# Optimization experiments

Measured on AMD Instinct MI355X. Metric: run time of the kernel, lower is better.

Reference implementation:

```python
import jax, jax.numpy as jnp
import numpy as np

B, N, GN, GS = 16, 100000, 4096, 64  # batch, points, num_groups, group_size


def setup_inputs() -> dict:
    key = jax.random.key(0)
    k1, k2, k3 = jax.random.split(key, 3)
    x_proto = jax.random.normal(k1, (B, N, 3), dtype=jnp.float32)
    template = jax.random.normal(k2, (N, 3), dtype=jnp.float32)
    groups = jax.random.randint(k3, (GN, GS), 0, N, dtype=jnp.int32)
    return {"x_proto": x_proto, "template": template, "groups": groups}


def reference(x_proto, template, groups):
    # x_proto: [B, N, 3], template: [N, 3], groups: [GN, GS] int indices
    b, n, _ = x_proto.shape
    Yg = template[groups]                      # [GN, GS, 3] gathered template
    Xg = x_proto[:, groups]                    # [B, GN, GS, 3] gathered current points

    # Kabsch: align template group Y to current X (R @ Y + t ~ X)
    muY = Yg.mean(axis=1)                      # [GN, 3]
    muX = Xg.mean(axis=2)                      # [B, GN, 3]
    Yc = Yg - muY[:, None, :]
    Xc = Xg - muX[:, :, None, :]
    H = jnp.einsum('gni,bgnj->bgij', Yc, Xc)   # [B, GN, 3, 3] covariance
    U, S, Vh = jnp.linalg.svd(H)
    V = jnp.swapaxes(Vh, -2, -1)
    R0 = V @ jnp.swapaxes(U, -2, -1)
    det = jnp.linalg.det(R0)                   # [B, GN]
    # flip last column of V where det < 0 to get a proper rotation
    s = jnp.where(det < 0, -1.0, 1.0).astype(x_proto.dtype)
    col_scale = jnp.stack([jnp.ones_like(s), jnp.ones_like(s), s], axis=-1)  # [B, GN, 3]
    R = (V * col_scale[..., None, :]) @ jnp.swapaxes(U, -2, -1)              # [B, GN, 3, 3]
    t = muX - jnp.einsum('bgij,gj->bgi', R, muY)                             # [B, GN, 3]

    # project template group through (R, t)
    Xg_proj = jnp.einsum('bgij,gnj->bgni', R, Yg) + t[:, :, None, :]         # [B, GN, GS, 3]

    # scatter-add with overlap counting, then average
    flat_idx = groups.reshape(-1)              # [GN*GS]
    out = jnp.zeros_like(x_proto).at[:, flat_idx].add(Xg_proj.reshape(b, -1, 3))
    counts = jnp.zeros((n,), dtype=x_proto.dtype).at[flat_idx].add(1.0)
    counts = jnp.maximum(counts, 1.0)
    return out / counts[None, :, None]
```

## Files before the change

kernel.cpp:

```cpp
#include <hip/hip_runtime.h>
#include <math.h>

static constexpr int BB = 16;
static constexpr int NN = 100000;
static constexpr int GN = 4096;
static constexpr int GS = 64;
static constexpr int NP = BB * GN;
static constexpr int NE = GN * GS;
static constexpr int NBLK = (NN + 255) / 256;

__device__ __forceinline__ float wsum64(float v) {
#pragma unroll
  for (int off = 32; off > 0; off >>= 1) v += __shfl_xor(v, off, 64);
  return v;
}

__global__ __launch_bounds__(256) void k_tpl(
    const float* __restrict__ tpl, const int* __restrict__ groups,
    float* __restrict__ Yg, float* __restrict__ GmY, int* __restrict__ cnt) {
  int g    = blockIdx.x * 4 + (threadIdx.x >> 6);
  int lane = threadIdx.x & 63;
  int idx = groups[g * GS + lane];
  atomicAdd(&cnt[idx], 1);
  float y0 = tpl[idx * 3 + 0], y1 = tpl[idx * 3 + 1], y2 = tpl[idx * 3 + 2];
  float* o = Yg + ((size_t)g * GS + lane) * 3;
  o[0] = y0; o[1] = y1; o[2] = y2;
  float sy0 = wsum64(y0), sy1 = wsum64(y1), sy2 = wsum64(y2);
  if (lane == 0) {
    const float inv = 1.0f / 64.0f;
    float4 m = make_float4(sy0 * inv, sy1 * inv, sy2 * inv, 0.0f);
    *(float4*)(GmY + (size_t)g * 4) = m;
  }
}

__global__ __launch_bounds__(256) void k_stats(
    const float* __restrict__ x, const float* __restrict__ Yg,
    const float* __restrict__ GmY, const int* __restrict__ groups,
    float* __restrict__ Ht) {
  int wid4 = blockIdx.x * 4 + (threadIdx.x >> 6);
  int lane = threadIdx.x & 63;
  int s    = lane >> 4;
  int l4   = lane & 15;
  int p = wid4 * 4 + s;
  int b = p >> 12;
  int g = p & (GN - 1);

  int4 iv = *(const int4*)(groups + (size_t)g * GS + l4 * 4);
  const float4* yv = (const float4*)(Yg + ((size_t)g * GS + l4 * 4) * 3);
  float4 ya = yv[0], yb = yv[1], yc = yv[2];

  const float* xb = x + (size_t)b * NN * 3;
  float sx0 = 0.f, sx1 = 0.f, sx2 = 0.f;
  float h00 = 0.f, h01 = 0.f, h02 = 0.f;
  float h10 = 0.f, h11 = 0.f, h12 = 0.f;
  float h20 = 0.f, h21 = 0.f, h22 = 0.f;

#define ACC(Y0, Y1, Y2, IDX)                                   \
  {                                                            \
    const float* xp = xb + (size_t)(IDX) * 3;                  \
    float x0 = xp[0], x1 = xp[1], x2 = xp[2];                  \
    sx0 += x0; sx1 += x1; sx2 += x2;                           \
    h00 += (Y0) * x0; h01 += (Y0) * x1; h02 += (Y0) * x2;      \
    h10 += (Y1) * x0; h11 += (Y1) * x1; h12 += (Y1) * x2;      \
    h20 += (Y2) * x0; h21 += (Y2) * x1; h22 += (Y2) * x2;      \
  }
  ACC(ya.x, ya.y, ya.z, iv.x);
  ACC(ya.w, yb.x, yb.y, iv.y);
  ACC(yb.z, yb.w, yc.x, iv.z);
  ACC(yc.y, yc.z, yc.w, iv.w);
#undef ACC

#define RED(V)                                                 \
  V += __shfl_xor(V, 8, 64); V += __shfl_xor(V, 4, 64);        \
  V += __shfl_xor(V, 2, 64); V += __shfl_xor(V, 1, 64);
  RED(sx0) RED(sx1) RED(sx2)
  RED(h00) RED(h01) RED(h02)
  RED(h10) RED(h11) RED(h12)
  RED(h20) RED(h21) RED(h22)
#undef RED

  if (l4 == 0) {
    const float inv = 1.0f / 64.0f;
    float4 m = *(const float4*)(GmY + (size_t)g * 4);
    float mx0 = sx0 * inv, mx1 = sx1 * inv, mx2 = sx2 * inv;
    float4 o0 = make_float4(mx0, mx1, mx2, h00 - m.x * sx0);
    float4 o1 = make_float4(h01 - m.x * sx1, h02 - m.x * sx2,
                            h10 - m.y * sx0, h11 - m.y * sx1);
    float4 o2 = make_float4(h12 - m.y * sx2, h20 - m.z * sx0,
                            h21 - m.z * sx1, h22 - m.z * sx2);
    float* o = Ht + (size_t)p * 12;
    *(float4*)(o + 0) = o0;
    *(float4*)(o + 4) = o1;
    *(float4*)(o + 8) = o2;
  }
}

#define JROT(P, Q, RR)                                                        \
  {                                                                           \
    float apq = K[P][Q];                                                      \
    if (fabsf(apq) > 1e-30f) {                                                \
      float app = K[P][P], aqq = K[Q][Q];                                     \
      float tau = (aqq - app) / (2.0f * apq);                                 \
      float tt = copysignf(1.0f, tau) / (fabsf(tau) + sqrtf(1.0f + tau*tau)); \
      float cc = 1.0f / sqrtf(1.0f + tt * tt);                                \
      float ss = tt * cc;                                                     \
      K[P][P] = app - tt * apq;                                               \
      K[Q][Q] = aqq + tt * apq;                                               \
      K[P][Q] = 0.0f; K[Q][P] = 0.0f;                                         \
      float krp = K[RR][P], krq = K[RR][Q];                                   \
      K[RR][P] = cc * krp - ss * krq; K[P][RR] = K[RR][P];                    \
      K[RR][Q] = ss * krp + cc * krq; K[Q][RR] = K[RR][Q];                    \
      float v0p = V[0][P], v0q = V[0][Q];                                     \
      float v1p = V[1][P], v1q = V[1][Q];                                     \
      float v2p = V[2][P], v2q = V[2][Q];                                     \
      V[0][P] = cc * v0p - ss * v0q; V[0][Q] = ss * v0p + cc * v0q;           \
      V[1][P] = cc * v1p - ss * v1q; V[1][Q] = ss * v1p + cc * v1q;           \
      V[2][P] = cc * v2p - ss * v2q; V[2][Q] = ss * v2p + cc * v2q;           \
    }                                                                         \
  }

#define FIN(AA, BBi, CC)                                                      \
  {                                                                           \
    float va0 = V[0][AA], va1 = V[1][AA], va2 = V[2][AA];                     \
    float vb0 = V[0][BBi], vb1 = V[1][BBi], vb2 = V[2][BBi];                  \
    float vc0 = V[0][CC], vc1 = V[1][CC], vc2 = V[2][CC];                     \
    float ua0 = A[0][0]*va0 + A[0][1]*va1 + A[0][2]*va2;                      \
    float ua1 = A[1][0]*va0 + A[1][1]*va1 + A[1][2]*va2;                      \
    float ua2 = A[2][0]*va0 + A[2][1]*va1 + A[2][2]*va2;                      \
    float il = 1.0f / sqrtf(ua0*ua0 + ua1*ua1 + ua2*ua2 + 1e-30f);            \
    ua0 *= il; ua1 *= il; ua2 *= il;                                          \
    float ub0 = A[0][0]*vb0 + A[0][1]*vb1 + A[0][2]*vb2;                      \
    float ub1 = A[1][0]*vb0 + A[1][1]*vb1 + A[1][2]*vb2;                      \
    float ub2 = A[2][0]*vb0 + A[2][1]*vb1 + A[2][2]*vb2;                      \
    il = 1.0f / sqrtf(ub0*ub0 + ub1*ub1 + ub2*ub2 + 1e-30f);                  \
    ub0 *= il; ub1 *= il; ub2 *= il;                                          \
    float dd = ua0*ub0 + ua1*ub1 + ua2*ub2;                                   \
    ub0 -= dd * ua0; ub1 -= dd * ua1; ub2 -= dd * ua2;                        \
    il = 1.0f / sqrtf(ub0*ub0 + ub1*ub1 + ub2*ub2 + 1e-30f);                  \
    ub0 *= il; ub1 *= il; ub2 *= il;                                          \
    float uc0 = ua1*ub2 - ua2*ub1;                                            \
    float uc1 = ua2*ub0 - ua0*ub2;                                            \
    float uc2 = ua0*ub1 - ua1*ub0;                                            \
    R[0][0] = va0*ua0 + vb0*ub0 + dsg*vc0*uc0;                                \
    R[0][1] = va0*ua1 + vb0*ub1 + dsg*vc0*uc1;                                \
    R[0][2] = va0*ua2 + vb0*ub2 + dsg*vc0*uc2;                                \
    R[1][0] = va1*ua0 + vb1*ub0 + dsg*vc1*uc0;                                \
    R[1][1] = va1*ua1 + vb1*ub1 + dsg*vc1*uc1;                                \
    R[1][2] = va1*ua2 + vb1*ub2 + dsg*vc1*uc2;                                \
    R[2][0] = va2*ua0 + vb2*ub0 + dsg*vc2*uc0;                                \
    R[2][1] = va2*ua1 + vb2*ub1 + dsg*vc2*uc1;                                \
    R[2][2] = va2*ua2 + vb2*ub2 + dsg*vc2*uc2;                                \
  }

__global__ __launch_bounds__(256) void k_svd(
    const float* __restrict__ Ht, const float* __restrict__ GmY,
    float* __restrict__ Rt) {
  int p = blockIdx.x * 256 + threadIdx.x;
  if (p >= NP) return;
  int g = p & (GN - 1);
  const float* h = Ht + (size_t)p * 12;
  float4 f0 = *(const float4*)(h + 0);
  float4 f1 = *(const float4*)(h + 4);
  float4 f2 = *(const float4*)(h + 8);
  float4 m  = *(const float4*)(GmY + (size_t)g * 4);
  float mx0 = f0.x, mx1 = f0.y, mx2 = f0.z;
  float my0 = m.x, my1 = m.y, my2 = m.z;
  float A[3][3];
  A[0][0] = f0.w; A[0][1] = f1.x; A[0][2] = f1.y;
  A[1][0] = f1.z; A[1][1] = f1.w; A[1][2] = f2.x;
  A[2][0] = f2.y; A[2][1] = f2.z; A[2][2] = f2.w;

  float K[3][3];
#pragma unroll
  for (int i = 0; i < 3; ++i)
#pragma unroll
    for (int j = 0; j < 3; ++j)
      K[i][j] = A[0][i]*A[0][j] + A[1][i]*A[1][j] + A[2][i]*A[2][j];

  float V[3][3] = {{1.f,0.f,0.f},{0.f,1.f,0.f},{0.f,0.f,1.f}};
#pragma unroll
  for (int sweep = 0; sweep < 5; ++sweep) {
    JROT(0, 1, 2);
    JROT(0, 2, 1);
    JROT(1, 2, 0);
  }

  float d0 = K[0][0], d1 = K[1][1], d2 = K[2][2];
  float detV = V[0][0]*(V[1][1]*V[2][2] - V[1][2]*V[2][1])
             - V[0][1]*(V[1][0]*V[2][2] - V[1][2]*V[2][0])
             + V[0][2]*(V[1][0]*V[2][1] - V[1][1]*V[2][0]);
  float dsg = (detV < 0.0f) ? -1.0f : 1.0f;

  float R[3][3];
  if (d0 <= d1 && d0 <= d2) {
    FIN(1, 2, 0);
  } else if (d1 <= d0 && d1 <= d2) {
    FIN(2, 0, 1);
  } else {
    FIN(0, 1, 2);
  }

  float t0 = mx0 - (R[0][0]*my0 + R[0][1]*my1 + R[0][2]*my2);
  float t1 = mx1 - (R[1][0]*my0 + R[1][1]*my1 + R[1][2]*my2);
  float t2 = mx2 - (R[2][0]*my0 + R[2][1]*my1 + R[2][2]*my2);

  float* o = Rt + (size_t)p * 12;
  o[0] = R[0][0]; o[1] = R[0][1]; o[2] = R[0][2];
  o[3] = R[1][0]; o[4] = R[1][1]; o[5] = R[1][2];
  o[6] = R[2][0]; o[7] = R[2][1]; o[8] = R[2][2];
  o[9] = t0; o[10] = t1; o[11] = t2;
}

__global__ __launch_bounds__(256) void k_scan1(
    const int* __restrict__ cnt, int* __restrict__ blockSums) {
  __shared__ int lds[4];
  int t = blockIdx.x * 256 + threadIdx.x;
  int v = (t < NN) ? cnt[t] : 0;
#pragma unroll
  for (int off = 32; off > 0; off >>= 1) v += __shfl_xor(v, off, 64);
  if ((threadIdx.x & 63) == 0) lds[threadIdx.x >> 6] = v;
  __syncthreads();
  if (threadIdx.x == 0)
    blockSums[blockIdx.x] = lds[0] + lds[1] + lds[2] + lds[3];
}

__global__ __launch_bounds__(512) void k_scan2(int* __restrict__ blockSums) {
  __shared__ int lds[512];
  int tid = threadIdx.x;
  int v = (tid < NBLK) ? blockSums[tid] : 0;
  lds[tid] = v;
  __syncthreads();
#pragma unroll
  for (int off = 1; off < 512; off <<= 1) {
    int add = (tid >= off) ? lds[tid - off] : 0;
    __syncthreads();
    lds[tid] += add;
    __syncthreads();
  }
  if (tid < NBLK) blockSums[tid] = lds[tid] - v;
}

__global__ __launch_bounds__(256) void k_scan3(
    const int* __restrict__ cnt, const int* __restrict__ blockSums,
    int* __restrict__ row_start, int* __restrict__ cursor) {
  __shared__ int lds[256];
  int tid = threadIdx.x;
  int t = blockIdx.x * 256 + tid;
  int v = (t < NN) ? cnt[t] : 0;
  lds[tid] = v;
  __syncthreads();
#pragma unroll
  for (int off = 1; off < 256; off <<= 1) {
    int add = (tid >= off) ? lds[tid - off] : 0;
    __syncthreads();
    lds[tid] += add;
    __syncthreads();
  }
  if (t < NN) {
    row_start[t] = lds[tid] - v + blockSums[blockIdx.x];
    cursor[t] = 0;
  }
}

__global__ __launch_bounds__(256) void k_fill(
    const int* __restrict__ groups, const int* __restrict__ row_start,
    int* __restrict__ cursor, unsigned* __restrict__ entries) {
  int e = blockIdx.x * 256 + threadIdx.x;
  if (e >= NE) return;
  int n = groups[e];
  int pos = atomicAdd(&cursor[n], 1);
  entries[row_start[n] + pos] = (unsigned)(e >> 6);
}

__global__ __launch_bounds__(256) void k_gather(
    const float* __restrict__ tpl, const int* __restrict__ row_start,
    const int* __restrict__ cnt, const unsigned* __restrict__ entries,
    const float* __restrict__ Rt, float* __restrict__ out) {
  int n = blockIdx.x * 256 + threadIdx.x;
  if (n >= NN) return;
  int b = blockIdx.y;
  int s = row_start[n];
  int c = cnt[n];
  float y0 = tpl[n * 3 + 0], y1 = tpl[n * 3 + 1], y2 = tpl[n * 3 + 2];
  float p0 = 0.f, p1 = 0.f, p2 = 0.f;
  for (int j = 0; j < c; ++j) {
    unsigned g = entries[s + j];
    const float* rt = Rt + ((size_t)b * GN + g) * 12;
    p0 += rt[0] * y0 + rt[1] * y1 + rt[2] * y2 + rt[9];
    p1 += rt[3] * y0 + rt[4] * y1 + rt[5] * y2 + rt[10];
    p2 += rt[6] * y0 + rt[7] * y1 + rt[8] * y2 + rt[11];
  }
  float inv = 1.0f / fmaxf((float)c, 1.0f);
  float* o = out + ((size_t)b * NN + (size_t)n) * 3;
  o[0] = p0 * inv;
  o[1] = p1 * inv;
  o[2] = p2 * inv;
}

extern "C" void kernel_launch(void* const* d_in, const int* in_sizes, int n_in,
                              void* d_out, int out_size, void* d_ws, size_t ws_size,
                              hipStream_t stream) {
  const float* x      = (const float*)d_in[0];
  const float* tpl    = (const float*)d_in[1];
  const int*   groups = (const int*)d_in[2];
  float* out = (float*)d_out;

  char* ws = (char*)d_ws;
  float* Yg        = (float*)ws;
  float* Rt        = (float*)ws;
  float* Ht        = (float*)(ws + (size_t)3 * 1024 * 1024);
  unsigned* entries= (unsigned*)(ws + (size_t)3 * 1024 * 1024);
  int* cursor      = (int*)(ws + (size_t)4 * 1024 * 1024);
  float* GmY       = (float*)(ws + (size_t)6 * 1024 * 1024);
  int* cnt         = (int*)(ws + (size_t)6 * 1024 * 1024 + 65536);
  int* row_start   = (int*)(ws + (size_t)6 * 1024 * 1024 + 65536 + 400000);
  int* blockSums   = (int*)(ws + (size_t)6 * 1024 * 1024 + 65536 + 800000);

  hipMemsetAsync(cnt, 0, (size_t)NN * sizeof(int), stream);

  k_tpl<<<GN / 4, 256, 0, stream>>>(tpl, groups, Yg, GmY, cnt);
  k_stats<<<NP / 16, 256, 0, stream>>>(x, Yg, GmY, groups, Ht);
  k_svd<<<NP / 256, 256, 0, stream>>>(Ht, GmY, Rt);
  k_scan1<<<NBLK, 256, 0, stream>>>(cnt, blockSums);
  k_scan2<<<1, 512, 0, stream>>>(blockSums);
  k_scan3<<<NBLK, 256, 0, stream>>>(cnt, blockSums, row_start, cursor);
  k_fill<<<NE / 256, 256, 0, stream>>>(groups, row_start, cursor, entries);
  k_gather<<<dim3(NBLK, BB), 256, 0, stream>>>(tpl, row_start, cnt, entries, Rt, out);
}
```

Before: 121.2 us.

## Replace CSR scan with fixed-slot lists, pad x to float4, split gather lanes

Builds per-point group lists directly in the template kernel using fixed 32-entry slots, removing the three scan kernels and the fill kernel. Adds a padding kernel that copies x into float4 layout (and zeroes counts) so the stats kernel does single aligned gathers, and remaps stats blocks across batches. The gather kernel now uses four lanes per point with float4 loads of R|t and a shuffle reduction. Costs an extra full pass over x and relies on no point appearing in more than 32 groups.

Result: faster. 118.0 us (-2.6%).

```diff
diff --git a/kernel.cpp b/kernel.cpp
--- a/kernel.cpp
+++ b/kernel.cpp
@@ -6,8 +6,7 @@
 static constexpr int GN = 4096;
 static constexpr int GS = 64;
 static constexpr int NP = BB * GN;
-static constexpr int NE = GN * GS;
-static constexpr int NBLK = (NN + 255) / 256;
+static constexpr int SLOT = 32;
 
 __device__ __forceinline__ float wsum64(float v) {
 #pragma unroll
@@ -15,29 +14,45 @@
   return v;
 }
 
+__global__ __launch_bounds__(256) void k_xpad(
+    const float4* __restrict__ x, float4* __restrict__ x4,
+    int4* __restrict__ cnt4) {
+  int t = blockIdx.x * 256 + threadIdx.x;
+  if (t < NN / 4) cnt4[t] = make_int4(0, 0, 0, 0);
+  if (t >= BB * NN / 4) return;
+  float4 a = x[t * 3 + 0], b = x[t * 3 + 1], c = x[t * 3 + 2];
+  x4[t * 4 + 0] = make_float4(a.x, a.y, a.z, 0.f);
+  x4[t * 4 + 1] = make_float4(a.w, b.x, b.y, 0.f);
+  x4[t * 4 + 2] = make_float4(b.z, b.w, c.x, 0.f);
+  x4[t * 4 + 3] = make_float4(c.y, c.z, c.w, 0.f);
+}
+
 __global__ __launch_bounds__(256) void k_tpl(
     const float* __restrict__ tpl, const int* __restrict__ groups,
-    float* __restrict__ Yg, float* __restrict__ GmY, int* __restrict__ cnt) {
+    float* __restrict__ Yg, float* __restrict__ GmY,
+    int* __restrict__ cnt, int* __restrict__ ent) {
   int g    = blockIdx.x * 4 + (threadIdx.x >> 6);
   int lane = threadIdx.x & 63;
   int idx = groups[g * GS + lane];
-  atomicAdd(&cnt[idx], 1);
+  int pos = atomicAdd(&cnt[idx], 1);
+  if (pos < SLOT) ent[idx * SLOT + pos] = g;
   float y0 = tpl[idx * 3 + 0], y1 = tpl[idx * 3 + 1], y2 = tpl[idx * 3 + 2];
   float* o = Yg + ((size_t)g * GS + lane) * 3;
   o[0] = y0; o[1] = y1; o[2] = y2;
   float sy0 = wsum64(y0), sy1 = wsum64(y1), sy2 = wsum64(y2);
   if (lane == 0) {
     const float inv = 1.0f / 64.0f;
-    float4 m = make_float4(sy0 * inv, sy1 * inv, sy2 * inv, 0.0f);
-    *(float4*)(GmY + (size_t)g * 4) = m;
+    *(float4*)(GmY + (size_t)g * 4) =
+        make_float4(sy0 * inv, sy1 * inv, sy2 * inv, 0.0f);
   }
 }
 
 __global__ __launch_bounds__(256) void k_stats(
-    const float* __restrict__ x, const float* __restrict__ Yg,
+    const float4* __restrict__ x4, const float* __restrict__ Yg,
     const float* __restrict__ GmY, const int* __restrict__ groups,
     float* __restrict__ Ht) {
-  int wid4 = blockIdx.x * 4 + (threadIdx.x >> 6);
+  int bid  = (blockIdx.x & 7) * 512 + (blockIdx.x >> 3);
+  int wid4 = bid * 4 + (threadIdx.x >> 6);
   int lane = threadIdx.x & 63;
   int s    = lane >> 4;
   int l4   = lane & 15;
@@ -49,7 +64,7 @@
   const float4* yv = (const float4*)(Yg + ((size_t)g * GS + l4 * 4) * 3);
   float4 ya = yv[0], yb = yv[1], yc = yv[2];
 
-  const float* xb = x + (size_t)b * NN * 3;
+  const float4* xb4 = x4 + (size_t)b * NN;
   float sx0 = 0.f, sx1 = 0.f, sx2 = 0.f;
   float h00 = 0.f, h01 = 0.f, h02 = 0.f;
   float h10 = 0.f, h11 = 0.f, h12 = 0.f;
@@ -57,12 +72,11 @@
 
 #define ACC(Y0, Y1, Y2, IDX)                                   \
   {                                                            \
-    const float* xp = xb + (size_t)(IDX) * 3;                  \
-    float x0 = xp[0], x1 = xp[1], x2 = xp[2];                  \
-    sx0 += x0; sx1 += x1; sx2 += x2;                           \
-    h00 += (Y0) * x0; h01 += (Y0) * x1; h02 += (Y0) * x2;      \
-    h10 += (Y1) * x0; h11 += (Y1) * x1; h12 += (Y1) * x2;      \
-    h20 += (Y2) * x0; h21 += (Y2) * x1; h22 += (Y2) * x2;      \
+    float4 xv = xb4[IDX];                                      \
+    sx0 += xv.x; sx1 += xv.y; sx2 += xv.z;                     \
+    h00 += (Y0) * xv.x; h01 += (Y0) * xv.y; h02 += (Y0) * xv.z;\
+    h10 += (Y1) * xv.x; h11 += (Y1) * xv.y; h12 += (Y1) * xv.z;\
+    h20 += (Y2) * xv.x; h21 += (Y2) * xv.y; h22 += (Y2) * xv.z;\
   }
   ACC(ya.x, ya.y, ya.z, iv.x);
   ACC(ya.w, yb.x, yb.y, iv.y);
@@ -211,90 +225,39 @@
   o[9] = t0; o[10] = t1; o[11] = t2;
 }
 
-__global__ __launch_bounds__(256) void k_scan1(
-    const int* __restrict__ cnt, int* __restrict__ blockSums) {
-  __shared__ int lds[4];
-  int t = blockIdx.x * 256 + threadIdx.x;
-  int v = (t < NN) ? cnt[t] : 0;
-#pragma unroll
-  for (int off = 32; off > 0; off >>= 1) v += __shfl_xor(v, off, 64);
-  if ((threadIdx.x & 63) == 0) lds[threadIdx.x >> 6] = v;
-  __syncthreads();
-  if (threadIdx.x == 0)
-    blockSums[blockIdx.x] = lds[0] + lds[1] + lds[2] + lds[3];
-}
-
-__global__ __launch_bounds__(512) void k_scan2(int* __restrict__ blockSums) {
-  __shared__ int lds[512];
-  int tid = threadIdx.x;
-  int v = (tid < NBLK) ? blockSums[tid] : 0;
-  lds[tid] = v;
-  __syncthreads();
-#pragma unroll
-  for (int off = 1; off < 512; off <<= 1) {
-    int add = (tid >= off) ? lds[tid - off] : 0;
-    __syncthreads();
-    lds[tid] += add;
-    __syncthreads();
-  }
-  if (tid < NBLK) blockSums[tid] = lds[tid] - v;
-}
-
-__global__ __launch_bounds__(256) void k_scan3(
-    const int* __restrict__ cnt, const int* __restrict__ blockSums,
-    int* __restrict__ row_start, int* __restrict__ cursor) {
-  __shared__ int lds[256];
-  int tid = threadIdx.x;
-  int t = blockIdx.x * 256 + tid;
-  int v = (t < NN) ? cnt[t] : 0;
-  lds[tid] = v;
-  __syncthreads();
-#pragma unroll
-  for (int off = 1; off < 256; off <<= 1) {
-    int add = (tid >= off) ? lds[tid - off] : 0;
-    __syncthreads();
-    lds[tid] += add;
-    __syncthreads();
-  }
-  if (t < NN) {
-    row_start[t] = lds[tid] - v + blockSums[blockIdx.x];
-    cursor[t] = 0;
-  }
-}
-
-__global__ __launch_bounds__(256) void k_fill(
-    const int* __restrict__ groups, const int* __restrict__ row_start,
-    int* __restrict__ cursor, unsigned* __restrict__ entries) {
-  int e = blockIdx.x * 256 + threadIdx.x;
-  if (e >= NE) return;
-  int n = groups[e];
-  int pos = atomicAdd(&cursor[n], 1);
-  entries[row_start[n] + pos] = (unsigned)(e >> 6);
-}
-
 __global__ __launch_bounds__(256) void k_gather(
-    const float* __restrict__ tpl, const int* __restrict__ row_start,
-    const int* __restrict__ cnt, const unsigned* __restrict__ entries,
-    const float* __restrict__ Rt, float* __restrict__ out) {
-  int n = blockIdx.x * 256 + threadIdx.x;
+    const float* __restrict__ tpl, const int* __restrict__ cnt,
+    const int* __restrict__ ent, const float* __restrict__ Rt,
+    float* __restrict__ out) {
+  int n  = blockIdx.x * 64 + (threadIdx.x >> 2);
+  int j0 = threadIdx.x & 3;
+  int b  = blockIdx.y;
   if (n >= NN) return;
-  int b = blockIdx.y;
-  int s = row_start[n];
-  int c = cnt[n];
+  int cn = cnt[n];
+  int c  = min(cn, SLOT);
   float y0 = tpl[n * 3 + 0], y1 = tpl[n * 3 + 1], y2 = tpl[n * 3 + 2];
   float p0 = 0.f, p1 = 0.f, p2 = 0.f;
-  for (int j = 0; j < c; ++j) {
-    unsigned g = entries[s + j];
-    const float* rt = Rt + ((size_t)b * GN + g) * 12;
-    p0 += rt[0] * y0 + rt[1] * y1 + rt[2] * y2 + rt[9];
-    p1 += rt[3] * y0 + rt[4] * y1 + rt[5] * y2 + rt[10];
-    p2 += rt[6] * y0 + rt[7] * y1 + rt[8] * y2 + rt[11];
-  }
-  float inv = 1.0f / fmaxf((float)c, 1.0f);
-  float* o = out + ((size_t)b * NN + (size_t)n) * 3;
-  o[0] = p0 * inv;
-  o[1] = p1 * inv;
-  o[2] = p2 * inv;
+  const float* Rb = Rt + (size_t)b * GN * 12;
+  for (int j = j0; j < c; j += 4) {
+    int g = ent[n * SLOT + j];
+    const float* rt = Rb + (size_t)g * 12;
+    float4 r0 = *(const float4*)(rt + 0);
+    float4 r1 = *(const float4*)(rt + 4);
+    float4 r2 = *(const float4*)(rt + 8);
+    p0 += r0.x * y0 + r0.y * y1 + r0.z * y2 + r2.y;
+    p1 += r0.w * y0 + r1.x * y1 + r1.y * y2 + r2.z;
+    p2 += r1.z * y0 + r1.w * y1 + r2.x * y2 + r2.w;
+  }
+  p0 += __shfl_xor(p0, 1, 64); p0 += __shfl_xor(p0, 2, 64);
+  p1 += __shfl_xor(p1, 1, 64); p1 += __shfl_xor(p1, 2, 64);
+  p2 += __shfl_xor(p2, 1, 64); p2 += __shfl_xor(p2, 2, 64);
+  if (j0 == 0) {
+    float inv = 1.0f / fmaxf((float)cn, 1.0f);
+    float* o = out + ((size_t)b * NN + (size_t)n) * 3;
+    o[0] = p0 * inv;
+    o[1] = p1 * inv;
+    o[2] = p2 * inv;
+  }
 }
 
 extern "C" void kernel_launch(void* const* d_in, const int* in_sizes, int n_in,
@@ -306,24 +269,24 @@
   float* out = (float*)d_out;
 
   char* ws = (char*)d_ws;
-  float* Yg        = (float*)ws;
-  float* Rt        = (float*)ws;
-  float* Ht        = (float*)(ws + (size_t)3 * 1024 * 1024);
-  unsigned* entries= (unsigned*)(ws + (size_t)3 * 1024 * 1024);
-  int* cursor      = (int*)(ws + (size_t)4 * 1024 * 1024);
-  float* GmY       = (float*)(ws + (size_t)6 * 1024 * 1024);
-  int* cnt         = (int*)(ws + (size_t)6 * 1024 * 1024 + 65536);
-  int* row_start   = (int*)(ws + (size_t)6 * 1024 * 1024 + 65536 + 400000);
-  int* blockSums   = (int*)(ws + (size_t)6 * 1024 * 1024 + 65536 + 800000);
-
-  hipMemsetAsync(cnt, 0, (size_t)NN * sizeof(int), stream);
-
-  k_tpl<<<GN / 4, 256, 0, stream>>>(tpl, groups, Yg, GmY, cnt);
-  k_stats<<<NP / 16, 256, 0, stream>>>(x, Yg, GmY, groups, Ht);
+  size_t o_x4  = 0;
+  size_t o_yg  = 25600000;
+  size_t o_ht  = o_yg + 3145728;
+  size_t o_gmy = o_ht + 3145728;
+  size_t o_cnt = o_gmy + 65536;
+  size_t o_ent = o_cnt + 400000;
+  float* x4   = (float*)(ws + o_x4);
+  float* Yg   = (float*)(ws + o_yg);
+  float* Rt   = (float*)(ws + o_yg);
+  float* Ht   = (float*)(ws + o_ht);
+  float* GmY  = (float*)(ws + o_gmy);
+  int*   cnt  = (int*)(ws + o_cnt);
+  int*   ent  = (int*)(ws + o_ent);
+
+  k_xpad<<<(BB * NN / 4 + 255) / 256, 256, 0, stream>>>(
+      (const float4*)x, (float4*)x4, (int4*)cnt);
+  k_tpl<<<GN / 4, 256, 0, stream>>>(tpl, groups, Yg, GmY, cnt, ent);
+  k_stats<<<NP / 16, 256, 0, stream>>>((const float4*)x4, Yg, GmY, groups, Ht);
   k_svd<<<NP / 256, 256, 0, stream>>>(Ht, GmY, Rt);
-  k_scan1<<<NBLK, 256, 0, stream>>>(cnt, blockSums);
-  k_scan2<<<1, 512, 0, stream>>>(blockSums);
-  k_scan3<<<NBLK, 256, 0, stream>>>(cnt, blockSums, row_start, cursor);
-  k_fill<<<NE / 256, 256, 0, stream>>>(groups, row_start, cursor, entries);
-  k_gather<<<dim3(NBLK, BB), 256, 0, stream>>>(tpl, row_start, cnt, entries, Rt, out);
-}
+  k_gather<<<dim3((NN + 63) / 64, BB), 256, 0, stream>>>(tpl, cnt, ent, Rt, out);
+}
```
